# Optimization experiments

Measured on AMD Instinct MI355X. Metric: run time of the kernel, lower is better.

The kernel has to match this reference:

```python
import jax, jax.numpy as jnp
import numpy as np

B, S, DM = 2, 2048, 1024
H, HD = 16, 64          # n_heads, head_dim
TPF = 128               # tokens_per_frame
NF = S // TPF           # n_frames
EPS = 1e-6
ROPE_THETA = 10000.0
NEG = -1e30  # stand-in for -inf that stays finite under softmax


def setup_inputs() -> dict:
    key = jax.random.key(0)
    ks = jax.random.split(key, 3)
    x = jax.random.normal(ks[0], (B, S, DM), dtype=jnp.float32)
    Wqkv = jax.random.normal(ks[1], (3 * DM, DM), dtype=jnp.float32) * (DM ** -0.5)
    bqkv = jnp.zeros((3 * DM,), dtype=jnp.float32)
    Wout = jax.random.normal(ks[2], (DM, DM), dtype=jnp.float32) * (DM ** -0.5)
    bout = jnp.zeros((DM,), dtype=jnp.float32)
    q_scale = jnp.ones((HD,), dtype=jnp.float32)
    k_scale = jnp.ones((HD,), dtype=jnp.float32)
    return {"x": x, "Wqkv": Wqkv, "bqkv": bqkv, "q_scale": q_scale,
            "k_scale": k_scale, "Wout": Wout, "bout": bout}


def _block_causal_mask(dtype):
    # Frame-block causal: query in frame i may attend keys in frames <= i.
    # Quirk from source: rows of the LAST frame additionally mask frame 0.
    fr = jnp.arange(S) // TPF
    allowed = fr[None, :] <= fr[:, None]
    quirk = (fr[:, None] == NF - 1) & (fr[None, :] == 0)
    allowed = allowed & ~quirk
    return jnp.where(allowed, jnp.zeros((), dtype), jnp.full((), NEG, dtype))


def _rmsnorm(t, scale):
    return t * jax.lax.rsqrt(jnp.mean(t * t, axis=-1, keepdims=True) + EPS) * scale


def _rope(t):
    # half-split rotary over flat token index; t: [B,H,S,D]
    pos = jnp.arange(S, dtype=jnp.float32)
    inv_freq = 1.0 / (ROPE_THETA ** (jnp.arange(0, HD, 2, dtype=jnp.float32) / HD))
    ang = pos[:, None] * inv_freq[None, :]              # [S, D/2]
    cos = jnp.concatenate([jnp.cos(ang), jnp.cos(ang)], axis=-1)  # [S, D]
    sin = jnp.concatenate([jnp.sin(ang), jnp.sin(ang)], axis=-1)
    t1, t2 = jnp.split(t, 2, axis=-1)
    rot = jnp.concatenate([-t2, t1], axis=-1)
    return t * cos + rot * sin


def reference(x, Wqkv, bqkv, q_scale, k_scale, Wout, bout):
    qkv = x @ Wqkv.T + bqkv                        # [B,S,3*DM]
    qkv = qkv.reshape(B, S, 3, H, HD)
    q, k, v = jnp.moveaxis(qkv, 2, 0)              # each [B,S,H,D]
    q = jnp.transpose(q, (0, 2, 1, 3))             # [B,H,S,D]
    k = jnp.transpose(k, (0, 2, 1, 3))
    v = jnp.transpose(v, (0, 2, 1, 3))
    q = _rmsnorm(q, q_scale)
    k = _rmsnorm(k, k_scale)
    q = _rope(q)
    k = _rope(k)
    mask = _block_causal_mask(x.dtype)             # [S,S]
    scores = jnp.einsum('bhqd,bhkd->bhqk', q, k) * (HD ** -0.5) + mask
    attn = jax.nn.softmax(scores, axis=-1)
    o = jnp.einsum('bhqk,bhkd->bhqd', attn, v)     # [B,H,S,D]
    o = jnp.transpose(o, (0, 2, 1, 3)).reshape(B, S, DM)
    return o @ Wout.T + bout
```

## Files before the change

kernel.cpp:

```cpp
#include <hip/hip_runtime.h>
#include <cstddef>
#include <cstdint>

constexpr int CB  = 2;
constexpr int CS  = 2048;
constexpr int CDM = 1024;
constexpr int CH  = 16;
constexpr int CHD = 64;
constexpr int CTPF = 128;
constexpr int CNF = 16;

typedef __attribute__((ext_vector_type(8))) short short8;
typedef __attribute__((ext_vector_type(4))) float f32x4;

__device__ inline ushort f32_bf16_rne(float x) {
  uint32_t u = __float_as_uint(x);
  u += 0x7FFFu + ((u >> 16) & 1u);
  return (ushort)(u >> 16);
}
__device__ inline float bf16_f32(ushort h) {
  return __uint_as_float(((uint32_t)h) << 16);
}
__device__ inline void split8(const float* v, short8& H, short8& L) {
#pragma unroll
  for (int j = 0; j < 8; ++j) {
    const ushort hh = f32_bf16_rne(v[j]);
    H[j] = (short)hh;
    L[j] = (short)f32_bf16_rne(v[j] - bf16_f32(hh));
  }
}

__global__ __launch_bounds__(256) void rope_tab(float2* __restrict__ T) {
  const int idx = blockIdx.x * 256 + threadIdx.x;
  const int s = idx >> 5;
  const int j = idx & 31;
  const float inv = powf(10000.0f, -(float)j * (1.0f / 32.0f));
  const float ang = (float)s * inv;
  T[idx] = make_float2(cosf(ang), sinf(ang));
}

__global__ __launch_bounds__(256) void split3(
    const float* __restrict__ s0, ushort* __restrict__ h0,
    ushort* __restrict__ l0, int n0,
    const float* __restrict__ s1, ushort* __restrict__ h1,
    ushort* __restrict__ l1, int n1,
    const float* __restrict__ s2, ushort* __restrict__ h2,
    ushort* __restrict__ l2, int n2) {
  const int ntot = n0 + n1 + n2;
  int i = blockIdx.x * 256 + threadIdx.x;
  const int stride = gridDim.x * 256;
  for (; i < ntot; i += stride) {
    const float* src;
    ushort *h, *l;
    int j = i;
    if (j < n0) {
      src = s0; h = h0; l = l0;
    } else if ((j -= n0) < n1) {
      src = s1; h = h1; l = l1;
    } else {
      j -= n1; src = s2; h = h2; l = l2;
    }
    float v[8];
    *(float4*)&v[0] = ((const float4*)src)[2 * j];
    *(float4*)&v[4] = ((const float4*)src)[2 * j + 1];
    short8 H, L;
    split8(v, H, L);
    *(short8*)&h[(size_t)j * 8] = H;
    *(short8*)&l[(size_t)j * 8] = L;
  }
}

__global__ __launch_bounds__(256) void gemm_ps(
    const ushort* __restrict__ Ah, const ushort* __restrict__ Al,
    const ushort* __restrict__ Bh, const ushort* __restrict__ Bl,
    const float* __restrict__ bias, float* __restrict__ C,
    int M, int N, int K) {
  __shared__ ushort As_h[128 * 32], As_l[128 * 32];
  __shared__ ushort Bs_h[128 * 32], Bs_l[128 * 32];
  const int tid = threadIdx.x;
  const int bm = blockIdx.y * 128;
  const int bn = blockIdx.x * 128;
  const int wid = tid >> 6;
  const int lane = tid & 63;
  const int wm = wid >> 1;
  const int wn = wid & 1;
  const int l15 = lane & 15;
  const int lk = lane >> 4;
  const int srow = tid >> 2;
  const int kq = (tid & 3) * 8;

  f32x4 acc[4][4];
#pragma unroll
  for (int i = 0; i < 4; ++i)
#pragma unroll
    for (int j = 0; j < 4; ++j) acc[i][j] = (f32x4){0.f, 0.f, 0.f, 0.f};

  for (int k0 = 0; k0 < K; k0 += 32) {
    __syncthreads();
#pragma unroll
    for (int c = 0; c < 2; ++c) {
      const int row = srow + c * 64;
      const int kg = kq ^ ((row & 6) << 2);
      const size_t ga = (size_t)(bm + row) * K + k0 + kg;
      const size_t gb = (size_t)(bn + row) * K + k0 + kg;
      const int lo = tid * 8 + c * 2048;
      __builtin_amdgcn_global_load_lds(
          (const __attribute__((address_space(1))) void*)(Ah + ga),
          (__attribute__((address_space(3))) void*)&As_h[lo], 16, 0, 0);
      __builtin_amdgcn_global_load_lds(
          (const __attribute__((address_space(1))) void*)(Al + ga),
          (__attribute__((address_space(3))) void*)&As_l[lo], 16, 0, 0);
      __builtin_amdgcn_global_load_lds(
          (const __attribute__((address_space(1))) void*)(Bh + gb),
          (__attribute__((address_space(3))) void*)&Bs_h[lo], 16, 0, 0);
      __builtin_amdgcn_global_load_lds(
          (const __attribute__((address_space(1))) void*)(Bl + gb),
          (__attribute__((address_space(3))) void*)&Bs_l[lo], 16, 0, 0);
    }
    __syncthreads();

    short8 ah[4], al[4], bh[4], bl[4];
#pragma unroll
    for (int fI = 0; fI < 4; ++fI) {
      const int ar = wm * 64 + fI * 16 + l15;
      const int aoff = ar * 32 + ((lk * 8) ^ ((ar & 6) << 2));
      ah[fI] = *(const short8*)&As_h[aoff];
      al[fI] = *(const short8*)&As_l[aoff];
      const int br = wn * 64 + fI * 16 + l15;
      const int boff = br * 32 + ((lk * 8) ^ ((br & 6) << 2));
      bh[fI] = *(const short8*)&Bs_h[boff];
      bl[fI] = *(const short8*)&Bs_l[boff];
    }
#pragma unroll
    for (int mf = 0; mf < 4; ++mf)
#pragma unroll
      for (int nf = 0; nf < 4; ++nf) {
        acc[mf][nf] = __builtin_amdgcn_mfma_f32_16x16x32_bf16(
            ah[mf], bh[nf], acc[mf][nf], 0, 0, 0);
        acc[mf][nf] = __builtin_amdgcn_mfma_f32_16x16x32_bf16(
            ah[mf], bl[nf], acc[mf][nf], 0, 0, 0);
        acc[mf][nf] = __builtin_amdgcn_mfma_f32_16x16x32_bf16(
            al[mf], bh[nf], acc[mf][nf], 0, 0, 0);
      }
  }

#pragma unroll
  for (int mf = 0; mf < 4; ++mf)
#pragma unroll
    for (int nf = 0; nf < 4; ++nf) {
      const int col = bn + wn * 64 + nf * 16 + l15;
      const int row0 = bm + wm * 64 + mf * 16 + lk * 4;
      const float bc = bias[col];
#pragma unroll
      for (int i = 0; i < 4; ++i)
        C[(size_t)(row0 + i) * N + col] = acc[mf][nf][i] + bc;
    }
}

__global__ __launch_bounds__(256) void qkv_prep(
    const float* __restrict__ qkv, const float* __restrict__ q_scale,
    const float* __restrict__ k_scale, const float2* __restrict__ Trig,
    ushort* __restrict__ Qh, ushort* __restrict__ Ql,
    ushort* __restrict__ Kh, ushort* __restrict__ Kl,
    ushort* __restrict__ Vth, ushort* __restrict__ Vtl) {
  __shared__ float Vtile[64][68];
  const int lane = threadIdx.x & 63;
  const int w = threadIdx.x >> 6;
  const int st = blockIdx.x;
  const int h = blockIdx.y;
  const int b = blockIdx.z;

  const float qs = q_scale[lane];
  const float ks = k_scale[lane];
  const int j = lane & 31;
  const float sgn = (lane < 32) ? -1.f : 1.f;

  for (int it = 0; it < 16; ++it) {
    const int sl = w * 16 + it;
    const int s = st * 64 + sl;
    const size_t row =
        ((size_t)(b * CS + s)) * (3 * CDM) + (size_t)h * CHD + lane;
    float qv = qkv[row];
    float kv = qkv[row + CDM];
    const float vv = qkv[row + 2 * CDM];

    float sq = qv * qv, sk2 = kv * kv;
#pragma unroll
    for (int off = 32; off > 0; off >>= 1) {
      sq += __shfl_xor(sq, off);
      sk2 += __shfl_xor(sk2, off);
    }
    qv *= rsqrtf(sq * (1.f / CHD) + 1e-6f) * qs;
    kv *= rsqrtf(sk2 * (1.f / CHD) + 1e-6f) * ks;

    const float2 cstab = Trig[s * 32 + j];
    const float cs = cstab.x;
    const float sn = cstab.y;
    const float qp = __shfl_xor(qv, 32);
    const float kp = __shfl_xor(kv, 32);
    const float qr = fmaf(qv, cs, sgn * qp * sn) * 0.125f;
    const float kr = fmaf(kv, cs, sgn * kp * sn);

    const size_t tok = ((size_t)(b * CH + h)) * CS + s;
    const size_t obq = tok * CHD + lane;
    const ushort qhh = f32_bf16_rne(qr);
    Qh[obq] = qhh;
    Ql[obq] = f32_bf16_rne(qr - bf16_f32(qhh));
    const size_t obk = tok * CHD + (lane ^ ((s & 7) << 3));
    const ushort khh = f32_bf16_rne(kr);
    Kh[obk] = khh;
    Kl[obk] = f32_bf16_rne(kr - bf16_f32(khh));
    Vtile[lane][sl] = vv;
  }
  __syncthreads();
  const int d = threadIdx.x >> 2;
  const int sq4 = (threadIdx.x & 3) * 16;
  const size_t vrow = (((size_t)(b * CH + h)) * CHD + d) * CS + st * 64;
  const int vmk = (d & 7) << 3;
#pragma unroll
  for (int j0 = 0; j0 < 16; j0 += 8) {
    float v8[8];
#pragma unroll
    for (int jj = 0; jj < 8; ++jj) v8[jj] = Vtile[d][sq4 + j0 + jj];
    short8 H, L;
    split8(v8, H, L);
    const int c0 = (sq4 + j0) ^ vmk;
    *(short8*)&Vth[vrow + c0] = H;
    *(short8*)&Vtl[vrow + c0] = L;
  }
}

__global__ __launch_bounds__(512, 4) void attn_fwd_mfma(
    const ushort* __restrict__ Qh, const ushort* __restrict__ Ql,
    const ushort* __restrict__ Kh, const ushort* __restrict__ Kl,
    const ushort* __restrict__ Vth, const ushort* __restrict__ Vtl,
    ushort* __restrict__ Oh, ushort* __restrict__ Ol) {
  __shared__ ushort Ks_h[64 * 64], Ks_l[64 * 64];
  __shared__ ushort Vs_h[64 * 64], Vs_l[64 * 64];
  __shared__ ushort Ps_h[128 * 64], Ps_l[128 * 64];
  const int tid = threadIdx.x;
  const int b = blockIdx.x;
  const int h = blockIdx.y;
  const int fsel = blockIdx.z;
  const int f = (fsel < 8) ? (15 - fsel) : (fsel - 8);
  const int lane = tid & 63;
  const int wid = tid >> 6;
  const int l15 = lane & 15;
  const int lk = lane >> 4;
  const int qb = wid * 16;
  const size_t hb = ((size_t)(b * CH + h)) * CS * CHD;
  const size_t vtb = ((size_t)(b * CH + h)) * CHD * CS;

  short8 qh[2], ql[2];
#pragma unroll
  for (int ks = 0; ks < 2; ++ks) {
    const size_t qoff = hb +
        (size_t)(f * CTPF + qb + l15) * CHD + ks * 32 + lk * 8;
    qh[ks] = *(const short8*)(Qh + qoff);
    ql[ks] = *(const short8*)(Ql + qoff);
  }

  f32x4 accO[4];
#pragma unroll
  for (int no = 0; no < 4; ++no) accO[no] = (f32x4){0.f, 0.f, 0.f, 0.f};
  float m = -1e30f;
  float lsum = 0.f;

  const int kf0 = (f == CNF - 1) ? 1 : 0;
  for (int kf = kf0; kf <= f; ++kf) {
#pragma unroll 1
    for (int half = 0; half < 2; ++half) {
      const int cb = kf * CTPF + half * 64;
      __syncthreads();
      {
        const size_t kc = hb + (size_t)cb * CHD;
        const int u = tid * 8;
        __builtin_amdgcn_global_load_lds(
            (const __attribute__((address_space(1))) void*)(Kh + kc + u),
            (__attribute__((address_space(3))) void*)&Ks_h[u], 16, 0, 0);
        __builtin_amdgcn_global_load_lds(
            (const __attribute__((address_space(1))) void*)(Kl + kc + u),
            (__attribute__((address_space(3))) void*)&Ks_l[u], 16, 0, 0);
        const size_t va = vtb + (size_t)(u >> 6) * CS + cb + (u & 63);
        __builtin_amdgcn_global_load_lds(
            (const __attribute__((address_space(1))) void*)(Vth + va),
            (__attribute__((address_space(3))) void*)&Vs_h[u], 16, 0, 0);
        __builtin_amdgcn_global_load_lds(
            (const __attribute__((address_space(1))) void*)(Vtl + va),
            (__attribute__((address_space(3))) void*)&Vs_l[u], 16, 0, 0);
      }
      __syncthreads();

      f32x4 sacc[4];
#pragma unroll
      for (int mf = 0; mf < 4; ++mf) sacc[mf] = (f32x4){0.f, 0.f, 0.f, 0.f};
#pragma unroll
      for (int ks = 0; ks < 2; ++ks) {
        short8 kh[4], kl[4];
#pragma unroll
        for (int mf = 0; mf < 4; ++mf) {
          const int krow = mf * 16 + l15;
          const int base = krow * 64 + ((ks * 32 + lk * 8) ^ ((krow & 7) << 3));
          kh[mf] = *(const short8*)&Ks_h[base];
          kl[mf] = *(const short8*)&Ks_l[base];
        }
#pragma unroll
        for (int mf = 0; mf < 4; ++mf) {
          sacc[mf] = __builtin_amdgcn_mfma_f32_16x16x32_bf16(
              kh[mf], qh[ks], sacc[mf], 0, 0, 0);
          sacc[mf] = __builtin_amdgcn_mfma_f32_16x16x32_bf16(
              kh[mf], ql[ks], sacc[mf], 0, 0, 0);
          sacc[mf] = __builtin_amdgcn_mfma_f32_16x16x32_bf16(
              kl[mf], qh[ks], sacc[mf], 0, 0, 0);
        }
      }

      float cm = sacc[0][0];
#pragma unroll
      for (int mf = 0; mf < 4; ++mf)
#pragma unroll
        for (int i = 0; i < 4; ++i) cm = fmaxf(cm, sacc[mf][i]);
      cm = fmaxf(cm, __shfl_xor(cm, 16));
      cm = fmaxf(cm, __shfl_xor(cm, 32));
      const float mn = fmaxf(m, cm);
      const float c = __expf(m - mn);
      m = mn;
      float ps = 0.f;
      const int qrow = qb + l15;
      const int qmk = (qrow & 7) << 3;
#pragma unroll
      for (int mf = 0; mf < 4; ++mf) {
        float p0 = __expf(sacc[mf][0] - mn);
        float p1 = __expf(sacc[mf][1] - mn);
        float p2 = __expf(sacc[mf][2] - mn);
        float p3 = __expf(sacc[mf][3] - mn);
        ps += (p0 + p1) + (p2 + p3);
        const ushort h0 = f32_bf16_rne(p0), h1 = f32_bf16_rne(p1);
        const ushort h2 = f32_bf16_rne(p2), h3 = f32_bf16_rne(p3);
        uint2 hw, lw;
        hw.x = (uint32_t)h0 | ((uint32_t)h1 << 16);
        hw.y = (uint32_t)h2 | ((uint32_t)h3 << 16);
        lw.x = (uint32_t)f32_bf16_rne(p0 - bf16_f32(h0)) |
               ((uint32_t)f32_bf16_rne(p1 - bf16_f32(h1)) << 16);
        lw.y = (uint32_t)f32_bf16_rne(p2 - bf16_f32(h2)) |
               ((uint32_t)f32_bf16_rne(p3 - bf16_f32(h3)) << 16);
        const int off = qrow * 64 + ((mf * 16 + lk * 4) ^ qmk);
        *(uint2*)&Ps_h[off] = hw;
        *(uint2*)&Ps_l[off] = lw;
      }
      ps += __shfl_xor(ps, 16);
      ps += __shfl_xor(ps, 32);
      lsum = lsum * c + ps;

#pragma unroll
      for (int i = 0; i < 4; ++i) {
        const float cq = __shfl(c, lk * 4 + i);
#pragma unroll
        for (int no = 0; no < 4; ++no) accO[no][i] *= cq;
      }

#pragma unroll
      for (int ks = 0; ks < 2; ++ks) {
        const int prow = qb + l15;
        const int pbase = prow * 64 + ((ks * 32 + lk * 8) ^ ((prow & 7) << 3));
        const short8 pa_h = *(const short8*)&Ps_h[pbase];
        const short8 pa_l = *(const short8*)&Ps_l[pbase];
        short8 vb_h[4], vb_l[4];
#pragma unroll
        for (int no = 0; no < 4; ++no) {
          const int vrow = no * 16 + l15;
          const int base = vrow * 64 + ((ks * 32 + lk * 8) ^ ((vrow & 7) << 3));
          vb_h[no] = *(const short8*)&Vs_h[base];
          vb_l[no] = *(const short8*)&Vs_l[base];
        }
#pragma unroll
        for (int no = 0; no < 4; ++no) {
          accO[no] = __builtin_amdgcn_mfma_f32_16x16x32_bf16(
              pa_h, vb_h[no], accO[no], 0, 0, 0);
          accO[no] = __builtin_amdgcn_mfma_f32_16x16x32_bf16(
              pa_h, vb_l[no], accO[no], 0, 0, 0);
          accO[no] = __builtin_amdgcn_mfma_f32_16x16x32_bf16(
              pa_l, vb_h[no], accO[no], 0, 0, 0);
        }
      }
    }
  }

  const float il = 1.f / lsum;
#pragma unroll
  for (int i = 0; i < 4; ++i) {
    const float wv = __shfl(il, lk * 4 + i);
    const int srow = f * CTPF + qb + lk * 4 + i;
    const size_t obase = (size_t)(b * CS + srow) * CDM + h * CHD;
#pragma unroll
    for (int no = 0; no < 4; ++no) {
      const float val = accO[no][i] * wv;
      const ushort hh = f32_bf16_rne(val);
      Oh[obase + no * 16 + l15] = hh;
      Ol[obase + no * 16 + l15] = f32_bf16_rne(val - bf16_f32(hh));
    }
  }
}

extern "C" void kernel_launch(void* const* d_in, const int* in_sizes, int n_in,
                              void* d_out, int out_size, void* d_ws, size_t ws_size,
                              hipStream_t stream) {
  const float* x       = (const float*)d_in[0];
  const float* Wqkv    = (const float*)d_in[1];
  const float* bqkv    = (const float*)d_in[2];
  const float* q_scale = (const float*)d_in[3];
  const float* k_scale = (const float*)d_in[4];
  const float* Wout    = (const float*)d_in[5];
  const float* bout    = (const float*)d_in[6];
  float* out = (float*)d_out;

  ushort* W = (ushort*)d_ws;
  const size_t qkvN = (size_t)(CB * CS) * (3 * CDM);
  const size_t perA = (size_t)CB * CH * CS * CHD;
  const size_t WqN  = (size_t)(3 * CDM) * CDM;
  const size_t WoN  = (size_t)CDM * CDM;

  float*  qkvF = (float*)W;
  ushort* Oh   = W;
  ushort* Ol   = W + perA;
  ushort* R1   = W + 2 * qkvN;
  ushort* Qh = R1;            ushort* Ql = R1 + perA;
  ushort* Kh = R1 + 2 * perA; ushort* Kl = R1 + 3 * perA;
  ushort* Vth = R1 + 4 * perA; ushort* Vtl = R1 + 5 * perA;
  ushort* xh  = R1;            ushort* xl  = R1 + perA;
  ushort* Wqh = R1 + 2 * perA; ushort* Wql = Wqh + WqN;
  ushort* Wouth = R1 + 6 * perA; ushort* Woutl = Wouth + WoN;
  float2* Trig = (float2*)(Woutl + WoN);

  rope_tab<<<256, 256, 0, stream>>>(Trig);
  split3<<<2048, 256, 0, stream>>>(x, xh, xl, (int)(perA / 8),
                                   Wqkv, Wqh, Wql, (int)(WqN / 8),
                                   Wout, Wouth, Woutl, (int)(WoN / 8));

  dim3 g1((3 * CDM) / 128, (CB * CS) / 128);
  gemm_ps<<<g1, 256, 0, stream>>>(xh, xl, Wqh, Wql, bqkv, qkvF,
                                  CB * CS, 3 * CDM, CDM);

  dim3 g2(CS / 64, CH, CB);
  qkv_prep<<<g2, 256, 0, stream>>>(qkvF, q_scale, k_scale, Trig,
                                   Qh, Ql, Kh, Kl, Vth, Vtl);

  dim3 g3(CB, CH, CNF);
  attn_fwd_mfma<<<g3, 512, 0, stream>>>(Qh, Ql, Kh, Kl, Vth, Vtl, Oh, Ol);

  dim3 g4(CDM / 128, (CB * CS) / 128);
  gemm_ps<<<g4, 256, 0, stream>>>(Oh, Ol, Wouth, Woutl, bout, out,
                                  CB * CS, CDM, CDM);
}
```

Before: 246.6 us.

## Double-buffer K/V tiles in LDS and pass P through registers via shuffles

The attention kernel now keeps two LDS buffers for K and V and issues the async global-to-LDS loads for the next 64-key chunk before computing on the current one, with one barrier per chunk instead of two. The P tile no longer goes through LDS. Each lane rebuilds its MFMA A-operand from the score accumulators with cross-lane shuffles. This aims to hide global load latency and cut LDS traffic and barriers, at the cost of more shuffle instructions and the same LDS footprint, which could affect occupancy.

```diff
diff --git a/kernel.cpp b/kernel.cpp
--- a/kernel.cpp
+++ b/kernel.cpp
@@ -12,6 +12,7 @@
 
 typedef __attribute__((ext_vector_type(8))) short short8;
 typedef __attribute__((ext_vector_type(4))) float f32x4;
+typedef __attribute__((ext_vector_type(4))) int i32x4;
 
 __device__ inline ushort f32_bf16_rne(float x) {
   uint32_t u = __float_as_uint(x);
@@ -235,19 +236,17 @@
     const ushort* __restrict__ Kh, const ushort* __restrict__ Kl,
     const ushort* __restrict__ Vth, const ushort* __restrict__ Vtl,
     ushort* __restrict__ Oh, ushort* __restrict__ Ol) {
-  __shared__ ushort Ks_h[64 * 64], Ks_l[64 * 64];
-  __shared__ ushort Vs_h[64 * 64], Vs_l[64 * 64];
-  __shared__ ushort Ps_h[128 * 64], Ps_l[128 * 64];
+  __shared__ ushort Ks_h[2 * 4096], Ks_l[2 * 4096];
+  __shared__ ushort Vs_h[2 * 4096], Vs_l[2 * 4096];
   const int tid = threadIdx.x;
   const int b = blockIdx.x;
   const int h = blockIdx.y;
   const int fsel = blockIdx.z;
   const int f = (fsel < 8) ? (15 - fsel) : (fsel - 8);
   const int lane = tid & 63;
-  const int wid = tid >> 6;
   const int l15 = lane & 15;
   const int lk = lane >> 4;
-  const int qb = wid * 16;
+  const int qb = (tid >> 6) * 16;
   const size_t hb = ((size_t)(b * CH + h)) * CS * CHD;
   const size_t vtb = ((size_t)(b * CH + h)) * CHD * CS;
 
@@ -267,123 +266,137 @@
   float lsum = 0.f;
 
   const int kf0 = (f == CNF - 1) ? 1 : 0;
-  for (int kf = kf0; kf <= f; ++kf) {
-#pragma unroll 1
-    for (int half = 0; half < 2; ++half) {
-      const int cb = kf * CTPF + half * 64;
-      __syncthreads();
-      {
-        const size_t kc = hb + (size_t)cb * CHD;
-        const int u = tid * 8;
-        __builtin_amdgcn_global_load_lds(
-            (const __attribute__((address_space(1))) void*)(Kh + kc + u),
-            (__attribute__((address_space(3))) void*)&Ks_h[u], 16, 0, 0);
-        __builtin_amdgcn_global_load_lds(
-            (const __attribute__((address_space(1))) void*)(Kl + kc + u),
-            (__attribute__((address_space(3))) void*)&Ks_l[u], 16, 0, 0);
-        const size_t va = vtb + (size_t)(u >> 6) * CS + cb + (u & 63);
-        __builtin_amdgcn_global_load_lds(
-            (const __attribute__((address_space(1))) void*)(Vth + va),
-            (__attribute__((address_space(3))) void*)&Vs_h[u], 16, 0, 0);
-        __builtin_amdgcn_global_load_lds(
-            (const __attribute__((address_space(1))) void*)(Vtl + va),
-            (__attribute__((address_space(3))) void*)&Vs_l[u], 16, 0, 0);
-      }
-      __syncthreads();
-
-      f32x4 sacc[4];
-#pragma unroll
-      for (int mf = 0; mf < 4; ++mf) sacc[mf] = (f32x4){0.f, 0.f, 0.f, 0.f};
-#pragma unroll
-      for (int ks = 0; ks < 2; ++ks) {
-        short8 kh[4], kl[4];
-#pragma unroll
-        for (int mf = 0; mf < 4; ++mf) {
-          const int krow = mf * 16 + l15;
-          const int base = krow * 64 + ((ks * 32 + lk * 8) ^ ((krow & 7) << 3));
-          kh[mf] = *(const short8*)&Ks_h[base];
-          kl[mf] = *(const short8*)&Ks_l[base];
-        }
-#pragma unroll
-        for (int mf = 0; mf < 4; ++mf) {
-          sacc[mf] = __builtin_amdgcn_mfma_f32_16x16x32_bf16(
-              kh[mf], qh[ks], sacc[mf], 0, 0, 0);
-          sacc[mf] = __builtin_amdgcn_mfma_f32_16x16x32_bf16(
-              kh[mf], ql[ks], sacc[mf], 0, 0, 0);
-          sacc[mf] = __builtin_amdgcn_mfma_f32_16x16x32_bf16(
-              kl[mf], qh[ks], sacc[mf], 0, 0, 0);
-        }
-      }
-
-      float cm = sacc[0][0];
-#pragma unroll
-      for (int mf = 0; mf < 4; ++mf)
-#pragma unroll
-        for (int i = 0; i < 4; ++i) cm = fmaxf(cm, sacc[mf][i]);
-      cm = fmaxf(cm, __shfl_xor(cm, 16));
-      cm = fmaxf(cm, __shfl_xor(cm, 32));
-      const float mn = fmaxf(m, cm);
-      const float c = __expf(m - mn);
-      m = mn;
-      float ps = 0.f;
-      const int qrow = qb + l15;
-      const int qmk = (qrow & 7) << 3;
+  const int nc = 2 * (f - kf0 + 1);
+
+  auto STAGE = [&](int ch, int buf) {
+    const int cb = (kf0 + (ch >> 1)) * CTPF + (ch & 1) * 64;
+    const size_t kc = hb + (size_t)cb * CHD;
+    const int u = tid * 8;
+    const int o = buf * 4096 + u;
+    __builtin_amdgcn_global_load_lds(
+        (const __attribute__((address_space(1))) void*)(Kh + kc + u),
+        (__attribute__((address_space(3))) void*)&Ks_h[o], 16, 0, 0);
+    __builtin_amdgcn_global_load_lds(
+        (const __attribute__((address_space(1))) void*)(Kl + kc + u),
+        (__attribute__((address_space(3))) void*)&Ks_l[o], 16, 0, 0);
+    const size_t va = vtb + (size_t)(u >> 6) * CS + cb + (u & 63);
+    __builtin_amdgcn_global_load_lds(
+        (const __attribute__((address_space(1))) void*)(Vth + va),
+        (__attribute__((address_space(3))) void*)&Vs_h[o], 16, 0, 0);
+    __builtin_amdgcn_global_load_lds(
+        (const __attribute__((address_space(1))) void*)(Vtl + va),
+        (__attribute__((address_space(3))) void*)&Vs_l[o], 16, 0, 0);
+  };
+
+  int cur = 0;
+  STAGE(0, 0);
+  __syncthreads();
+
+  for (int ch = 0; ch < nc; ++ch) {
+    if (ch + 1 < nc) STAGE(ch + 1, cur ^ 1);
+    const int kb = cur * 4096;
+
+    f32x4 sacc[4];
+#pragma unroll
+    for (int mf = 0; mf < 4; ++mf) sacc[mf] = (f32x4){0.f, 0.f, 0.f, 0.f};
+#pragma unroll
+    for (int ks = 0; ks < 2; ++ks) {
+      short8 kh[4], kl[4];
 #pragma unroll
       for (int mf = 0; mf < 4; ++mf) {
-        float p0 = __expf(sacc[mf][0] - mn);
-        float p1 = __expf(sacc[mf][1] - mn);
-        float p2 = __expf(sacc[mf][2] - mn);
-        float p3 = __expf(sacc[mf][3] - mn);
-        ps += (p0 + p1) + (p2 + p3);
-        const ushort h0 = f32_bf16_rne(p0), h1 = f32_bf16_rne(p1);
-        const ushort h2 = f32_bf16_rne(p2), h3 = f32_bf16_rne(p3);
-        uint2 hw, lw;
-        hw.x = (uint32_t)h0 | ((uint32_t)h1 << 16);
-        hw.y = (uint32_t)h2 | ((uint32_t)h3 << 16);
-        lw.x = (uint32_t)f32_bf16_rne(p0 - bf16_f32(h0)) |
-               ((uint32_t)f32_bf16_rne(p1 - bf16_f32(h1)) << 16);
-        lw.y = (uint32_t)f32_bf16_rne(p2 - bf16_f32(h2)) |
-               ((uint32_t)f32_bf16_rne(p3 - bf16_f32(h3)) << 16);
-        const int off = qrow * 64 + ((mf * 16 + lk * 4) ^ qmk);
-        *(uint2*)&Ps_h[off] = hw;
-        *(uint2*)&Ps_l[off] = lw;
-      }
-      ps += __shfl_xor(ps, 16);
-      ps += __shfl_xor(ps, 32);
-      lsum = lsum * c + ps;
-
-#pragma unroll
-      for (int i = 0; i < 4; ++i) {
-        const float cq = __shfl(c, lk * 4 + i);
-#pragma unroll
-        for (int no = 0; no < 4; ++no) accO[no][i] *= cq;
-      }
-
-#pragma unroll
-      for (int ks = 0; ks < 2; ++ks) {
-        const int prow = qb + l15;
-        const int pbase = prow * 64 + ((ks * 32 + lk * 8) ^ ((prow & 7) << 3));
-        const short8 pa_h = *(const short8*)&Ps_h[pbase];
-        const short8 pa_l = *(const short8*)&Ps_l[pbase];
-        short8 vb_h[4], vb_l[4];
-#pragma unroll
-        for (int no = 0; no < 4; ++no) {
-          const int vrow = no * 16 + l15;
-          const int base = vrow * 64 + ((ks * 32 + lk * 8) ^ ((vrow & 7) << 3));
-          vb_h[no] = *(const short8*)&Vs_h[base];
-          vb_l[no] = *(const short8*)&Vs_l[base];
-        }
-#pragma unroll
-        for (int no = 0; no < 4; ++no) {
-          accO[no] = __builtin_amdgcn_mfma_f32_16x16x32_bf16(
-              pa_h, vb_h[no], accO[no], 0, 0, 0);
-          accO[no] = __builtin_amdgcn_mfma_f32_16x16x32_bf16(
-              pa_h, vb_l[no], accO[no], 0, 0, 0);
-          accO[no] = __builtin_amdgcn_mfma_f32_16x16x32_bf16(
-              pa_l, vb_h[no], accO[no], 0, 0, 0);
-        }
-      }
-    }
+        const int krow = mf * 16 + l15;
+        const int base =
+            kb + krow * 64 + ((ks * 32 + lk * 8) ^ ((krow & 7) << 3));
+        kh[mf] = *(const short8*)&Ks_h[base];
+        kl[mf] = *(const short8*)&Ks_l[base];
+      }
+#pragma unroll
+      for (int mf = 0; mf < 4; ++mf) {
+        sacc[mf] = __builtin_amdgcn_mfma_f32_16x16x32_bf16(
+            kh[mf], qh[ks], sacc[mf], 0, 0, 0);
+        sacc[mf] = __builtin_amdgcn_mfma_f32_16x16x32_bf16(
+            kh[mf], ql[ks], sacc[mf], 0, 0, 0);
+        sacc[mf] = __builtin_amdgcn_mfma_f32_16x16x32_bf16(
+            kl[mf], qh[ks], sacc[mf], 0, 0, 0);
+      }
+    }
+
+    float cm = sacc[0][0];
+#pragma unroll
+    for (int mf = 0; mf < 4; ++mf)
+#pragma unroll
+      for (int i = 0; i < 4; ++i) cm = fmaxf(cm, sacc[mf][i]);
+    cm = fmaxf(cm, __shfl_xor(cm, 16));
+    cm = fmaxf(cm, __shfl_xor(cm, 32));
+    const float mn = fmaxf(m, cm);
+    const float cexp = __expf(m - mn);
+    m = mn;
+    float ps = 0.f;
+    int ph[4][2], pl[4][2];
+#pragma unroll
+    for (int mf = 0; mf < 4; ++mf) {
+      float p0 = __expf(sacc[mf][0] - mn);
+      float p1 = __expf(sacc[mf][1] - mn);
+      float p2 = __expf(sacc[mf][2] - mn);
+      float p3 = __expf(sacc[mf][3] - mn);
+      ps += (p0 + p1) + (p2 + p3);
+      const ushort h0 = f32_bf16_rne(p0), h1 = f32_bf16_rne(p1);
+      const ushort h2 = f32_bf16_rne(p2), h3 = f32_bf16_rne(p3);
+      ph[mf][0] = (int)((uint32_t)h0 | ((uint32_t)h1 << 16));
+      ph[mf][1] = (int)((uint32_t)h2 | ((uint32_t)h3 << 16));
+      pl[mf][0] = (int)((uint32_t)f32_bf16_rne(p0 - bf16_f32(h0)) |
+                        ((uint32_t)f32_bf16_rne(p1 - bf16_f32(h1)) << 16));
+      pl[mf][1] = (int)((uint32_t)f32_bf16_rne(p2 - bf16_f32(h2)) |
+                        ((uint32_t)f32_bf16_rne(p3 - bf16_f32(h3)) << 16));
+    }
+    ps += __shfl_xor(ps, 16);
+    ps += __shfl_xor(ps, 32);
+    lsum = lsum * cexp + ps;
+
+#pragma unroll
+    for (int i = 0; i < 4; ++i) {
+      const float cq = __shfl(cexp, lk * 4 + i);
+#pragma unroll
+      for (int no = 0; no < 4; ++no) accO[no][i] *= cq;
+    }
+
+#pragma unroll
+    for (int ks = 0; ks < 2; ++ks) {
+      i32x4 wa_h, wa_l;
+#pragma unroll
+      for (int t = 0; t < 4; ++t) {
+        const int srcLane = l15 + 16 * ((2 * lk + (t >> 1)) & 3);
+        const int a_h = __shfl(ph[2 * ks][t & 1], srcLane);
+        const int b_h = __shfl(ph[2 * ks + 1][t & 1], srcLane);
+        wa_h[t] = (lk >= 2) ? b_h : a_h;
+        const int a_l = __shfl(pl[2 * ks][t & 1], srcLane);
+        const int b_l = __shfl(pl[2 * ks + 1][t & 1], srcLane);
+        wa_l[t] = (lk >= 2) ? b_l : a_l;
+      }
+      const short8 pa_h = __builtin_bit_cast(short8, wa_h);
+      const short8 pa_l = __builtin_bit_cast(short8, wa_l);
+      short8 vb_h[4], vb_l[4];
+#pragma unroll
+      for (int no = 0; no < 4; ++no) {
+        const int vrow = no * 16 + l15;
+        const int base =
+            kb + vrow * 64 + ((ks * 32 + lk * 8) ^ ((vrow & 7) << 3));
+        vb_h[no] = *(const short8*)&Vs_h[base];
+        vb_l[no] = *(const short8*)&Vs_l[base];
+      }
+#pragma unroll
+      for (int no = 0; no < 4; ++no) {
+        accO[no] = __builtin_amdgcn_mfma_f32_16x16x32_bf16(
+            pa_h, vb_h[no], accO[no], 0, 0, 0);
+        accO[no] = __builtin_amdgcn_mfma_f32_16x16x32_bf16(
+            pa_h, vb_l[no], accO[no], 0, 0, 0);
+        accO[no] = __builtin_amdgcn_mfma_f32_16x16x32_bf16(
+            pa_l, vb_h[no], accO[no], 0, 0, 0);
+      }
+    }
+
+    __syncthreads();
+    cur ^= 1;
   }
 
   const float il = 1.f / lsum;
```

After: 254.1 us. 1.03x slower.
